# Kernel tuning notes

Hardware: AMD Instinct MI355X
Metric: run time of the kernel (lower is better)

The kernel has to match this reference:

```python
import jax, jax.numpy as jnp
import numpy as np

B, S, D = 32, 2048, 128


def setup_inputs() -> dict:
    key = jax.random.key(0)
    kq, kk, kv, km = jax.random.split(key, 4)
    queries = jax.random.normal(kq, (B, S, D), dtype=jnp.float32)
    keys = jax.random.normal(kk, (B, S, D), dtype=jnp.float32)
    values = jax.random.normal(kv, (B, S, D), dtype=jnp.float32)
    attention_mask = jax.random.randint(km, (B, S, S), 0, 2, dtype=jnp.int32)
    return {"queries": queries, "keys": keys, "values": values,
            "attention_mask": attention_mask}


def reference(queries, keys, values, attention_mask):
    d = queries.shape[-1]
    # scores: [B, S, S]
    scores = jnp.einsum("bqd,bkd->bqk", queries, keys) / jnp.sqrt(
        jnp.asarray(d, queries.dtype))
    scores = jnp.where(attention_mask == 0, jnp.asarray(-1e6, scores.dtype), scores)
    attn = jax.nn.softmax(scores, axis=-1)
    # dropout prob is 0.0 (eval-equivalent), so no dropout applied
    return jnp.einsum("bqk,bkd->bqd", attn, values)
```

## Files before the change

### kernel.cpp

```cpp
#include <hip/hip_runtime.h>

#define B_ 32
#define S_ 2048
#define D_ 128
#define NT 32
#define QB 128

typedef __bf16 bf16;
typedef unsigned u32;
typedef unsigned long long u64;
typedef __attribute__((ext_vector_type(8))) __bf16 bf16x8;
typedef __attribute__((ext_vector_type(16))) float f32x16;

__device__ __forceinline__ f32x16 mfma32(bf16x8 a, bf16x8 b, f32x16 c) {
  return __builtin_amdgcn_mfma_f32_32x32x16_bf16(a, b, c, 0, 0, 0);
}

__device__ __forceinline__ u32 pk2(bf16 a, bf16 b) {
  unsigned short ua = __builtin_bit_cast(unsigned short, a);
  unsigned short ub = __builtin_bit_cast(unsigned short, b);
  return (u32)ua | ((u32)ub << 16);
}

__device__ __forceinline__ void glds16(const bf16* g, char* l) {
  __builtin_amdgcn_global_load_lds(
      (const __attribute__((address_space(1))) void*)g,
      (__attribute__((address_space(3))) void*)l, 16, 0, 0);
}

__global__ __launch_bounds__(256) void k_prepass(const float* __restrict__ K,
                                                 bf16* __restrict__ khi,
                                                 bf16* __restrict__ klo) {
  const int bid = blockIdx.x;
  const int t = threadIdx.x;
  const int kr = t >> 2;
  const int cbase = (t & 3) * 4;
  const float* src = K + (size_t)bid * 8192 + kr * 128;
  bf16* ho = khi + (size_t)bid * 8192 + kr * 128;
  bf16* lo = klo + (size_t)bid * 8192 + kr * 128;
  const int swz = kr & 15;
#pragma unroll
  for (int j = 0; j < 4; ++j) {
    const int c = cbase + j;
    float4 a = *(const float4*)(src + c * 8);
    float4 b2 = *(const float4*)(src + c * 8 + 4);
    float f[8] = {a.x, a.y, a.z, a.w, b2.x, b2.y, b2.z, b2.w};
    bf16x8 h8, l8;
#pragma unroll
    for (int e = 0; e < 8; ++e) {
      bf16 hi = (bf16)f[e];
      h8[e] = hi;
      l8[e] = (bf16)(f[e] - (float)hi);
    }
    *(bf16x8*)(ho + (c ^ swz) * 8) = h8;
    *(bf16x8*)(lo + (c ^ swz) * 8) = l8;
  }
}

__global__ __launch_bounds__(256) void vt_prepass(const float* __restrict__ V,
                                                  bf16* __restrict__ vthi,
                                                  bf16* __restrict__ vtlo) {
  const int bid = blockIdx.x;
  const int b = bid >> 5, kt = bid & 31;
  const int kbase = kt * 64;
  const int t = threadIdx.x;
  __shared__ u32 Tpk[128][67];

  {
    const int dc = t & 31, kr0 = t >> 5;
#pragma unroll
    for (int i = 0; i < 8; ++i) {
      const int kr = kr0 + i * 8;
      float4 v = *(const float4*)(V + ((size_t)b * S_ + kbase + kr) * D_ + dc * 4);
      float f[4] = {v.x, v.y, v.z, v.w};
#pragma unroll
      for (int j = 0; j < 4; ++j) {
        bf16 hi = (bf16)f[j];
        bf16 lo = (bf16)(f[j] - (float)hi);
        Tpk[dc * 4 + j][kr] = pk2(hi, lo);
      }
    }
  }
  __syncthreads();
#pragma unroll
  for (int p = 0; p < 4; ++p) {
    const int g = p * 256 + t;
    const int d = g >> 3, c = g & 7;
    const int cs = c ^ (d & 7);
    u32 wv[8];
#pragma unroll
    for (int e = 0; e < 8; ++e) wv[e] = Tpk[d][cs * 8 + e];
    uint4 hi4, lo4;
    u32* hp = (u32*)&hi4;
    u32* lp = (u32*)&lo4;
#pragma unroll
    for (int j = 0; j < 4; ++j) {
      hp[j] = (wv[2 * j] & 0xffffu) | (wv[2 * j + 1] << 16);
      lp[j] = (wv[2 * j] >> 16) | (wv[2 * j + 1] & 0xffff0000u);
    }
    const size_t base = ((size_t)(b * NT + kt) * 128 + d) * 64 + c * 8;
    *(uint4*)(vthi + base) = hi4;
    *(uint4*)(vtlo + base) = lo4;
  }
}

__global__ __launch_bounds__(256, 2) void attn_kernel(
    const float* __restrict__ Q, const int* __restrict__ M,
    const bf16* __restrict__ khi_g, const bf16* __restrict__ klo_g,
    const bf16* __restrict__ vthi_g, const bf16* __restrict__ vtlo_g,
    float* __restrict__ Out) {
  extern __shared__ char smem[];
  const int t = threadIdx.x;
  const int w = t >> 6;
  const int lane = t & 63;
  const int i31 = t & 31;
  const int h = (t >> 5) & 1;

  const int bid = blockIdx.x;
  const int idx = bid >> 3;
  const int b = (bid & 7) * 4 + (idx >> 4);
  const int qbase = (idx & 15) * QB;
  const int qloc = w * 32 + i31;

  const float sc = 0.08838834764831843f * 1.4426950408889634f;
  bf16x8 qh[8], ql[8];
  {
    const float* qsrc = Q + ((size_t)b * S_ + qbase + qloc) * D_;
#pragma unroll
    for (int ds = 0; ds < 8; ++ds) {
      const int d0 = ds * 16 + h * 8;
      float4 a = *(const float4*)(qsrc + d0);
      float4 c = *(const float4*)(qsrc + d0 + 4);
      float f[8] = {a.x, a.y, a.z, a.w, c.x, c.y, c.z, c.w};
#pragma unroll
      for (int e = 0; e < 8; ++e) {
        float v = f[e] * sc;
        bf16 hi = (bf16)v;
        qh[ds][e] = hi;
        ql[ds][e] = (bf16)(v - (float)hi);
      }
    }
  }

  f32x16 acc[4];
#pragma unroll
  for (int dt = 0; dt < 4; ++dt)
#pragma unroll
    for (int e = 0; e < 16; ++e) acc[dt][e] = 0.f;
  float m_run = -3.0e38f, l_run = 0.f;

  const bf16* g0 = (w & 2) ? vthi_g : khi_g;
  const bf16* g1 = (w & 2) ? vtlo_g : klo_g;
  const bf16* gsel = (w & 1) ? g1 : g0;
  const size_t tstride = 8192;
  const bf16* gsrc0 = gsel + (size_t)(b * NT) * tstride + lane * 8;
  char* ldst = smem + w * 16384;

  const int* mptr = M + ((size_t)b * S_ + qbase + w * 32) * S_ + lane;

#pragma unroll
  for (int i = 0; i < 16; ++i) glds16(gsrc0 + i * 512, ldst + i * 1024);
  int mv[32];
#pragma unroll
  for (int r = 0; r < 32; ++r) mv[r] = mptr[r * S_];
  __syncthreads();

  for (int kt = 0; kt < NT; ++kt) {
    u64 mc = 0;
#pragma unroll
    for (int r = 0; r < 32; ++r) {
      const u64 bal = __ballot(mv[r] != 0);
      if (i31 == r) mc = bal;
    }
    {
      const int knb = ((kt + 1 < NT) ? kt + 1 : kt) * 64;
#pragma unroll
      for (int r = 0; r < 32; ++r) mv[r] = mptr[r * S_ + knb];
    }

    f32x16 s[2];
#pragma unroll
    for (int ct = 0; ct < 2; ++ct)
#pragma unroll
      for (int e = 0; e < 16; ++e) s[ct][e] = 0.f;
    __builtin_amdgcn_s_setprio(1);
#pragma unroll
    for (int ct = 0; ct < 2; ++ct) {
      const u32 rowb = (u32)(ct * 32 + i31) * 256;
      const u32 sw = (u32)(i31 & 15);
#pragma unroll
      for (int ds = 0; ds < 8; ++ds) {
        const u32 off = rowb + (((u32)(ds * 2 + h) ^ sw) * 16);
        bf16x8 kh = *(const bf16x8*)(smem + off);
        bf16x8 kl = *(const bf16x8*)(smem + 16384 + off);
        s[ct] = mfma32(kh, qh[ds], s[ct]);
        s[ct] = mfma32(kl, qh[ds], s[ct]);
        s[ct] = mfma32(kh, ql[ds], s[ct]);
      }
    }
    __builtin_amdgcn_s_setprio(0);

    float mx = -3.0e38f;
#pragma unroll
    for (int ct = 0; ct < 2; ++ct)
#pragma unroll
      for (int r = 0; r < 16; ++r) mx = fmaxf(mx, s[ct][r]);
    mx = fmaxf(mx, __shfl_xor(mx, 32, 64));
    const float m_new = fmaxf(m_run, mx);
    const float alpha = exp2f(m_run - m_new);
    const u32 mw0 = (u32)mc, mw1 = (u32)(mc >> 32);
    float rs = 0.f;
#pragma unroll
    for (int ct = 0; ct < 2; ++ct) {
      const u32 mword = ct ? mw1 : mw0;
#pragma unroll
      for (int r = 0; r < 16; ++r) {
        const int pos = (r & 3) + 8 * (r >> 2) + 4 * h;
        float p = exp2f(s[ct][r] - m_new);
        p = ((mword >> pos) & 1u) ? p : 0.f;
        s[ct][r] = p;
        rs += p;
      }
    }
    rs += __shfl_xor(rs, 32, 64);
    l_run = l_run * alpha + rs;
    m_run = m_new;
#pragma unroll
    for (int dt = 0; dt < 4; ++dt) acc[dt] = acc[dt] * alpha;

    __builtin_amdgcn_s_setprio(1);
#pragma unroll
    for (int ks = 0; ks < 4; ++ks) {
      const int ct = ks >> 1;
      const int a0 = (ks & 1) * 8;
      u32 PKh[4], PKl[4];
#pragma unroll
      for (int y = 0; y < 4; ++y) {
        const float p0 = s[ct][a0 + 2 * y];
        const float p1 = s[ct][a0 + 2 * y + 1];
        bf16 h0 = (bf16)p0, h1 = (bf16)p1;
        PKh[y] = pk2(h0, h1);
        PKl[y] = pk2((bf16)(p0 - (float)h0), (bf16)(p1 - (float)h1));
      }
      const u32 s0h = h ? PKh[0] : PKh[2];
      const u32 s1h = h ? PKh[1] : PKh[3];
      const u32 s0l = h ? PKl[0] : PKl[2];
      const u32 s1l = h ? PKl[1] : PKl[3];
      const u32 r0h = __shfl_xor(s0h, 32, 64);
      const u32 r1h = __shfl_xor(s1h, 32, 64);
      const u32 r0l = __shfl_xor(s0l, 32, 64);
      const u32 r1l = __shfl_xor(s1l, 32, 64);
      uint4 fh, fl;
      fh.x = h ? r0h : PKh[0];
      fh.y = h ? r1h : PKh[1];
      fh.z = h ? PKh[2] : r0h;
      fh.w = h ? PKh[3] : r1h;
      fl.x = h ? r0l : PKl[0];
      fl.y = h ? r1l : PKl[1];
      fl.z = h ? PKl[2] : r0l;
      fl.w = h ? PKl[3] : r1l;
      bf16x8 pah = __builtin_bit_cast(bf16x8, fh);
      bf16x8 pal = __builtin_bit_cast(bf16x8, fl);
#pragma unroll
      for (int dt = 0; dt < 4; ++dt) {
        const u32 d = (u32)(dt * 32 + i31);
        const u32 off = d * 128 + ((((u32)(ks * 2 + h)) ^ (d & 7)) * 16);
        bf16x8 vh = *(const bf16x8*)(smem + 32768 + off);
        bf16x8 vl = *(const bf16x8*)(smem + 49152 + off);
        acc[dt] = mfma32(vh, pah, acc[dt]);
        acc[dt] = mfma32(vh, pal, acc[dt]);
        acc[dt] = mfma32(vl, pah, acc[dt]);
      }
    }
    __builtin_amdgcn_s_setprio(0);

    __syncthreads();
    if (kt + 1 < NT) {
      const bf16* gsrc = gsrc0 + (size_t)(kt + 1) * tstride;
#pragma unroll
      for (int i = 0; i < 16; ++i) glds16(gsrc + i * 512, ldst + i * 1024);
    }
    __syncthreads();
  }

  const float inv_l = 1.0f / l_run;
  float* orow = Out + ((size_t)b * S_ + qbase + qloc) * D_;
#pragma unroll
  for (int dt = 0; dt < 4; ++dt) {
#pragma unroll
    for (int rr = 0; rr < 4; ++rr) {
      float4 o;
      o.x = acc[dt][rr * 4 + 0] * inv_l;
      o.y = acc[dt][rr * 4 + 1] * inv_l;
      o.z = acc[dt][rr * 4 + 2] * inv_l;
      o.w = acc[dt][rr * 4 + 3] * inv_l;
      *(float4*)(orow + dt * 32 + rr * 8 + h * 4) = o;
    }
  }
}

extern "C" void kernel_launch(void* const* d_in, const int* in_sizes, int n_in,
                              void* d_out, int out_size, void* d_ws,
                              size_t ws_size, hipStream_t stream) {
  (void)in_sizes; (void)n_in; (void)out_size; (void)ws_size;
  const float* Q = (const float*)d_in[0];
  const float* K = (const float*)d_in[1];
  const float* V = (const float*)d_in[2];
  const int* M = (const int*)d_in[3];
  float* Out = (float*)d_out;

  const size_t el = (size_t)B_ * S_ * D_;
  bf16* khi = (bf16*)d_ws;
  bf16* klo = khi + el;
  bf16* vthi = klo + el;
  bf16* vtlo = vthi + el;

  static int attr_set = 0;
  if (!attr_set) {
    hipFuncSetAttribute((const void*)attn_kernel,
                        hipFuncAttributeMaxDynamicSharedMemorySize, 65536);
    attr_set = 1;
  }

  k_prepass<<<dim3(B_ * NT), dim3(256), 0, stream>>>(K, khi, klo);
  vt_prepass<<<dim3(B_ * NT), dim3(256), 0, stream>>>(V, vthi, vtlo);
  attn_kernel<<<dim3(512), dim3(256), 65536, stream>>>(Q, M, khi, klo, vthi,
                                                       vtlo, Out);
}
```

Baseline: 868.9 us.

## Double-buffer K/V tiles in LDS with 256-query blocks of eight waves

Doubles the query block to 256 rows and the block size to 512 threads, so each K/V tile loaded into LDS is shared by twice as many queries. The LDS footprint grows to 128 KB, split into two buffers. The next tile's loads are issued into the alternate buffer before the current tile is computed, leaving one barrier per iteration instead of two. Mask loads now happen at the start of each iteration rather than being prefetched one tile ahead, which may expose more global-load latency. The larger LDS footprint also limits each CU to a single block.

Result: slower. 886.7 us (+2.1%).

```diff
diff --git a/kernel.cpp b/kernel.cpp
--- a/kernel.cpp
+++ b/kernel.cpp
@@ -4,7 +4,7 @@
 #define S_ 2048
 #define D_ 128
 #define NT 32
-#define QB 128
+#define QB 256
 
 typedef __bf16 bf16;
 typedef unsigned u32;
@@ -104,7 +104,7 @@
   }
 }
 
-__global__ __launch_bounds__(256, 2) void attn_kernel(
+__global__ __launch_bounds__(512, 2) void attn_kernel(
     const float* __restrict__ Q, const int* __restrict__ M,
     const bf16* __restrict__ khi_g, const bf16* __restrict__ klo_g,
     const bf16* __restrict__ vthi_g, const bf16* __restrict__ vtlo_g,
@@ -117,9 +117,9 @@
   const int h = (t >> 5) & 1;
 
   const int bid = blockIdx.x;
-  const int idx = bid >> 3;
-  const int b = (bid & 7) * 4 + (idx >> 4);
-  const int qbase = (idx & 15) * QB;
+  const int slot = bid >> 3;
+  const int b = (bid & 7) * 4 + (slot >> 3);
+  const int qbase = (slot & 7) * QB;
   const int qloc = w * 32 + i31;
 
   const float sc = 0.08838834764831843f * 1.4426950408889634f;
@@ -149,56 +149,64 @@
     for (int e = 0; e < 16; ++e) acc[dt][e] = 0.f;
   float m_run = -3.0e38f, l_run = 0.f;
 
-  const bf16* g0 = (w & 2) ? vthi_g : khi_g;
-  const bf16* g1 = (w & 2) ? vtlo_g : klo_g;
-  const bf16* gsel = (w & 1) ? g1 : g0;
-  const size_t tstride = 8192;
-  const bf16* gsrc0 = gsel + (size_t)(b * NT) * tstride + lane * 8;
-  char* ldst = smem + w * 16384;
+  const int reg = w >> 1, half = w & 1;
+  const bf16* gsel = (reg == 0) ? khi_g : (reg == 1) ? klo_g
+                     : (reg == 2) ? vthi_g : vtlo_g;
+  const bf16* gsrc0 = gsel + (size_t)(b * NT) * 8192 + half * 4096 + lane * 8;
+  const u32 lbase = (u32)(reg * 16384 + half * 8192);
 
   const int* mptr = M + ((size_t)b * S_ + qbase + w * 32) * S_ + lane;
 
 #pragma unroll
-  for (int i = 0; i < 16; ++i) glds16(gsrc0 + i * 512, ldst + i * 1024);
-  int mv[32];
-#pragma unroll
-  for (int r = 0; r < 32; ++r) mv[r] = mptr[r * S_];
+  for (int i = 0; i < 8; ++i) glds16(gsrc0 + i * 512, smem + lbase + i * 1024);
   __syncthreads();
 
+#pragma unroll 1
   for (int kt = 0; kt < NT; ++kt) {
+    const int cb = kt & 1;
+    const char* kb = smem + cb * 65536;
+
+    int mv[32];
+    {
+      const int knb = kt * 64;
+#pragma unroll
+      for (int r = 0; r < 32; ++r) mv[r] = mptr[r * S_ + knb];
+    }
+    if (kt + 1 < NT) {
+      const bf16* gsrc = gsrc0 + (size_t)(kt + 1) * 8192;
+      char* ldst = smem + (cb ^ 1) * 65536 + lbase;
+#pragma unroll
+      for (int i = 0; i < 8; ++i) glds16(gsrc + i * 512, ldst + i * 1024);
+    }
+
+    f32x16 s[2];
+#pragma unroll
+    for (int ct = 0; ct < 2; ++ct)
+#pragma unroll
+      for (int e = 0; e < 16; ++e) s[ct][e] = 0.f;
+    __builtin_amdgcn_s_setprio(1);
+#pragma unroll
+    for (int ct = 0; ct < 2; ++ct) {
+      const u32 rowb = (u32)(ct * 32 + i31) * 256;
+      const u32 sw = (u32)(i31 & 15);
+#pragma unroll
+      for (int ds = 0; ds < 8; ++ds) {
+        const u32 off = rowb + (((u32)(ds * 2 + h) ^ sw) * 16);
+        bf16x8 kh = *(const bf16x8*)(kb + off);
+        bf16x8 kl = *(const bf16x8*)(kb + 16384 + off);
+        s[ct] = mfma32(kh, qh[ds], s[ct]);
+        s[ct] = mfma32(kl, qh[ds], s[ct]);
+        s[ct] = mfma32(kh, ql[ds], s[ct]);
+      }
+    }
+    __builtin_amdgcn_s_setprio(0);
+
     u64 mc = 0;
 #pragma unroll
     for (int r = 0; r < 32; ++r) {
       const u64 bal = __ballot(mv[r] != 0);
       if (i31 == r) mc = bal;
     }
-    {
-      const int knb = ((kt + 1 < NT) ? kt + 1 : kt) * 64;
-#pragma unroll
-      for (int r = 0; r < 32; ++r) mv[r] = mptr[r * S_ + knb];
-    }
-
-    f32x16 s[2];
-#pragma unroll
-    for (int ct = 0; ct < 2; ++ct)
-#pragma unroll
-      for (int e = 0; e < 16; ++e) s[ct][e] = 0.f;
-    __builtin_amdgcn_s_setprio(1);
-#pragma unroll
-    for (int ct = 0; ct < 2; ++ct) {
-      const u32 rowb = (u32)(ct * 32 + i31) * 256;
-      const u32 sw = (u32)(i31 & 15);
-#pragma unroll
-      for (int ds = 0; ds < 8; ++ds) {
-        const u32 off = rowb + (((u32)(ds * 2 + h) ^ sw) * 16);
-        bf16x8 kh = *(const bf16x8*)(smem + off);
-        bf16x8 kl = *(const bf16x8*)(smem + 16384 + off);
-        s[ct] = mfma32(kh, qh[ds], s[ct]);
-        s[ct] = mfma32(kl, qh[ds], s[ct]);
-        s[ct] = mfma32(kh, ql[ds], s[ct]);
-      }
-    }
-    __builtin_amdgcn_s_setprio(0);
 
     float mx = -3.0e38f;
 #pragma unroll
@@ -265,8 +273,8 @@
       for (int dt = 0; dt < 4; ++dt) {
         const u32 d = (u32)(dt * 32 + i31);
         const u32 off = d * 128 + ((((u32)(ks * 2 + h)) ^ (d & 7)) * 16);
-        bf16x8 vh = *(const bf16x8*)(smem + 32768 + off);
-        bf16x8 vl = *(const bf16x8*)(smem + 49152 + off);
+        bf16x8 vh = *(const bf16x8*)(kb + 32768 + off);
+        bf16x8 vl = *(const bf16x8*)(kb + 49152 + off);
         acc[dt] = mfma32(vh, pah, acc[dt]);
         acc[dt] = mfma32(vh, pal, acc[dt]);
         acc[dt] = mfma32(vl, pah, acc[dt]);
@@ -274,12 +282,6 @@
     }
     __builtin_amdgcn_s_setprio(0);
 
-    __syncthreads();
-    if (kt + 1 < NT) {
-      const bf16* gsrc = gsrc0 + (size_t)(kt + 1) * tstride;
-#pragma unroll
-      for (int i = 0; i < 16; ++i) glds16(gsrc + i * 512, ldst + i * 1024);
-    }
     __syncthreads();
   }
 
@@ -318,12 +320,12 @@
   static int attr_set = 0;
   if (!attr_set) {
     hipFuncSetAttribute((const void*)attn_kernel,
-                        hipFuncAttributeMaxDynamicSharedMemorySize, 65536);
+                        hipFuncAttributeMaxDynamicSharedMemorySize, 131072);
     attr_set = 1;
   }
 
   k_prepass<<<dim3(B_ * NT), dim3(256), 0, stream>>>(K, khi, klo);
   vt_prepass<<<dim3(B_ * NT), dim3(256), 0, stream>>>(V, vthi, vtlo);
-  attn_kernel<<<dim3(512), dim3(256), 65536, stream>>>(Q, M, khi, klo, vthi,
-                                                       vtlo, Out);
-}
+  attn_kernel<<<dim3(256), dim3(512), 131072, stream>>>(Q, M, khi, klo, vthi,
+                                                        vtlo, Out);
+}
```
